# Kernel optimization log

Measured on AMD Instinct MI355X. Metric: run time of the kernel, lower is better.

Reference implementation:

```python
import jax, jax.numpy as jnp
import numpy as np
import math

L = 6      # num transformer layers
D = 128    # hidden_dim
H = 8      # heads
C = D // H # per-head dim (concat -> H*C == hidden_dim so residual add works)
F = 9      # node_features
OUT = 3    # output_dim
B, S, NN = 2, 128, 64
N = B * S * NN
E = 262144


def setup_inputs() -> dict:
    key = jax.random.key(0)
    ks = jax.random.split(key, 16)
    sc = 0.02
    g = lambda k, shp: jax.random.normal(k, shp, jnp.float32) * sc

    x = jax.random.normal(ks[0], (N, F), jnp.float32)
    edge_index = jax.random.randint(ks[1], (2, E), 0, N, dtype=jnp.int32)

    # sinusoidal positional encoding buffer [S, D]
    pos = np.arange(S, dtype=np.float32)[:, None]
    div = np.exp(np.arange(0, D, 2, dtype=np.float32) * (-math.log(10000.0) / D))
    pe = np.zeros((S, D), np.float32)
    pe[:, 0::2] = np.sin(pos * div)
    pe[:, 1::2] = np.cos(pos * div)

    return dict(
        x=x, edge_index=edge_index, pe=jnp.asarray(pe),
        Win=g(ks[2], (F, D)), bin_=jnp.zeros((D,), jnp.float32),
        Wq=g(ks[3], (L, D, D)), bq=jnp.zeros((L, D), jnp.float32),
        Wk=g(ks[4], (L, D, D)), bk=jnp.zeros((L, D), jnp.float32),
        Wv=g(ks[5], (L, D, D)), bv=jnp.zeros((L, D), jnp.float32),
        Ws=g(ks[6], (L, D, D)), bs=jnp.zeros((L, D), jnp.float32),
        Wb=g(ks[7], (L, 3 * D, 1)), bb=jnp.zeros((L, 1), jnp.float32),
        ln_g=jnp.ones((L, D), jnp.float32), ln_b=jnp.zeros((L, D), jnp.float32),
        Wo1=g(ks[8], (D, D // 2)), bo1=jnp.zeros((D // 2,), jnp.float32),
        Wo2=g(ks[9], (D // 2, OUT)), bo2=jnp.zeros((OUT,), jnp.float32),
        batch_size=B, seq_len=S, num_nodes=NN,
    )


def _layer_norm(x, g, b, eps=1e-5):
    mu = x.mean(-1, keepdims=True)
    var = ((x - mu) ** 2).mean(-1, keepdims=True)
    return (x - mu) / jnp.sqrt(var + eps) * g + b


def _transformer_conv(h, src, dst, Wq, bq, Wk, bk, Wv, bv, Ws, bs, Wb, bb):
    # PyG TransformerConv (beta=True, concat): edge gather -> per-head dot scores
    # -> scatter-softmax over incoming edges per dst node -> scatter-add aggregate.
    n = h.shape[0]
    q = (h @ Wq + bq).reshape(n, H, C)
    k = (h @ Wk + bk).reshape(n, H, C)
    v = (h @ Wv + bv).reshape(n, H, C)
    scores = jnp.einsum('ehc,ehc->eh', q[dst], k[src]) / math.sqrt(C)  # [E,H]
    m = jax.ops.segment_max(scores, dst, num_segments=n)               # [N,H]
    ex = jnp.exp(scores - jax.lax.stop_gradient(m)[dst])
    denom = jax.ops.segment_sum(ex, dst, num_segments=n)
    alpha = ex / (denom[dst] + 1e-16)                                  # [E,H]
    msg = (v[src] * alpha[:, :, None]).reshape(-1, H * C)              # [E,D]
    agg = jax.ops.segment_sum(msg, dst, num_segments=n)                # [N,D]
    xr = h @ Ws + bs                                                   # skip branch
    beta = jax.nn.sigmoid(jnp.concatenate([agg, xr, agg - xr], -1) @ Wb + bb)
    return beta * xr + (1.0 - beta) * agg


def reference(x, edge_index, pe, Win, bin_, Wq, bq, Wk, bk, Wv, bv, Ws, bs,
              Wb, bb, ln_g, ln_b, Wo1, bo1, Wo2, bo2,
              batch_size, seq_len, num_nodes):
    src, dst = edge_index[0], edge_index[1]
    d = Win.shape[1]
    h = x @ Win + bin_
    # add temporal positional encoding per timestep
    h = (h.reshape(batch_size, seq_len, num_nodes, d)
         + pe[:seq_len][None, :, None, :]).reshape(-1, d)
    for i in range(Wq.shape[0]):
        hn = _transformer_conv(h, src, dst, Wq[i], bq[i], Wk[i], bk[i],
                               Wv[i], bv[i], Ws[i], bs[i], Wb[i], bb[i])
        h = _layer_norm(h + hn, ln_g[i], ln_b[i])
    return jax.nn.relu(h @ Wo1 + bo1) @ Wo2 + bo2
```

## Files before the change

kernel.cpp:

```cpp
#include <hip/hip_runtime.h>

#define NNODES 16384
#define EDGES  262144
#define DH     128
#define NH     8
#define CH     16
#define NL     6
#define SEQ    128
#define NNPG   64

#define PBLK   768
#define PTHR   (PBLK * 256)
#define PWAV   (PBLK * 4)

typedef short bf16x8 __attribute__((ext_vector_type(8)));
typedef float f32x4 __attribute__((ext_vector_type(4)));
typedef float f32x2 __attribute__((ext_vector_type(2)));

static __device__ __forceinline__ unsigned short f2bf(float f) {
  unsigned u = __float_as_uint(f);
  u += 0x7FFFu + ((u >> 16) & 1u);
  return (unsigned short)(u >> 16);
}
static __device__ __forceinline__ float bfl(unsigned u) { return __uint_as_float(u << 16); }
static __device__ __forceinline__ float bfh(unsigned u) { return __uint_as_float(u & 0xffff0000u); }
static __device__ __forceinline__ f32x2 mk2(float x, float y) { f32x2 t; t[0] = x; t[1] = y; return t; }

__global__ __launch_bounds__(256) void k_pro(const int* __restrict__ ei,
    int* __restrict__ cnt, int* __restrict__ csr_pad,
    const float* __restrict__ Wq, const float* __restrict__ Wk,
    const float* __restrict__ Wv, const float* __restrict__ Ws,
    unsigned short* __restrict__ Wf,
    const float* __restrict__ x, const float* __restrict__ Win,
    const float* __restrict__ bin, const float* __restrict__ pe,
    float* __restrict__ h, unsigned short* __restrict__ hb) {
  const int tid = threadIdx.x;
  const int lane = tid & 63, wid = tid >> 6;
  const int gtid = blockIdx.x * 256 + tid;
  const int gw = blockIdx.x * 4 + wid;

  for (int e = gtid; e < EDGES; e += PTHR) {
    const int d = ei[EDGES + e];
    const int s = ei[e];
    const int slot = atomicAdd(&cnt[d], 1);
    if (slot < 64) csr_pad[d * 64 + (slot & 7) * 8 + (slot >> 3)] = s;
  }

  if (gw < NL * 128) {
    const int layer = gw >> 7, rem = gw & 127;
    const int mat = rem >> 5, tile = rem & 31;
    const int nt = tile >> 2, kt = tile & 3;
    const float* W = ((mat == 0) ? Wq : (mat == 1) ? Wk : (mat == 2) ? Wv : Ws)
                     + layer * DH * DH;
    const int nn = nt * 16 + (lane & 15);
    const int k0 = kt * 32 + (lane >> 4) * 8;
    unsigned pk[4];
#pragma unroll
    for (int jj = 0; jj < 4; ++jj) {
      const unsigned lo = f2bf(W[(k0 + 2 * jj) * DH + nn]);
      const unsigned hi = f2bf(W[(k0 + 2 * jj + 1) * DH + nn]);
      pk[jj] = lo | (hi << 16);
    }
    uint4 o = {pk[0], pk[1], pk[2], pk[3]};
    *(uint4*)&Wf[(((layer * 4 + mat) * 32 + tile) * 64 + lane) * 8] = o;
  }

  for (int n = gw; n < NNODES; n += PWAV) {
    const int d0 = lane * 2;
    float xs[9];
#pragma unroll
    for (int f = 0; f < 9; ++f) xs[f] = x[n * 9 + f];
    float a0 = bin[d0], a1 = bin[d0 + 1];
#pragma unroll
    for (int f = 0; f < 9; ++f) {
      const float2 w = *(const float2*)&Win[f * DH + d0];
      a0 = fmaf(xs[f], w.x, a0);
      a1 = fmaf(xs[f], w.y, a1);
    }
    const float2 pev = *(const float2*)&pe[((n / NNPG) % SEQ) * DH + d0];
    const float v0 = a0 + pev.x, v1 = a1 + pev.y;
    float2 hv = {v0, v1};
    *(float2*)&h[n * DH + d0] = hv;
    *(unsigned*)&hb[n * DH + d0] = (unsigned)f2bf(v0) | ((unsigned)f2bf(v1) << 16);
  }
}

__global__ __launch_bounds__(512, 2) void k_gemm(const unsigned short* __restrict__ hb,
    const unsigned short* __restrict__ Wf,
    const float* __restrict__ bq, const float* __restrict__ bk,
    const float* __restrict__ bv, const float* __restrict__ bs,
    unsigned short* __restrict__ qb, unsigned char* __restrict__ kv8,
    float* __restrict__ xr) {
  __shared__ uint4 As4[512];
  const int mt = blockIdx.x;
  const int wv = threadIdx.x >> 6, lane = threadIdx.x & 63;
  {
    const int t = threadIdx.x;
    const int row = t >> 4, cb = t & 15;
    As4[t] = *(const uint4*)&hb[(mt * 32 + row) * DH + ((cb ^ (row & 7)) * 8)];
  }
  __syncthreads();

  const int g = wv;
  const int mat = g >> 1, nbase = (g & 1) * 64;
  const unsigned short* Wm = Wf + mat * 16384;
  const float* bias = (mat == 0) ? bq : (mat == 1) ? bk : (mat == 2) ? bv : bs;
  const int m0 = lane & 15, quad = lane >> 4;
  const int nt0 = (g & 1) * 4;
  const char* Asb = (const char*)As4;

  const f32x4 z = {0.f, 0.f, 0.f, 0.f};
  f32x4 acc[2][4] = {{z, z, z, z}, {z, z, z, z}};
#pragma unroll
  for (int kt = 0; kt < 4; ++kt) {
    const int cbr = kt * 4 + quad;
    const bf16x8 a0 = *(const bf16x8*)(Asb + m0 * 256 + ((cbr ^ (m0 & 7)) * 16));
    const bf16x8 a1 = *(const bf16x8*)(Asb + (16 + m0) * 256 + ((cbr ^ (m0 & 7)) * 16));
#pragma unroll
    for (int j = 0; j < 4; ++j) {
      const bf16x8 b = *(const bf16x8*)&Wm[(((nt0 + j) * 4 + kt) * 64 + lane) * 8];
      acc[0][j] = __builtin_amdgcn_mfma_f32_16x16x32_bf16(a0, b, acc[0][j], 0, 0, 0);
      acc[1][j] = __builtin_amdgcn_mfma_f32_16x16x32_bf16(a1, b, acc[1][j], 0, 0, 0);
    }
  }
  const int kvoff = (mat == 1) ? 0 : 16;
#pragma unroll
  for (int half = 0; half < 2; ++half) {
#pragma unroll
    for (int j = 0; j < 4; ++j) {
      const int col = nbase + j * 16 + m0;
      const float bvv = bias[col];
#pragma unroll
      for (int r = 0; r < 4; ++r) {
        const float val = acc[half][j][r] + bvv;
        const int row = mt * 32 + half * 16 + quad * 4 + r;
        if (mat == 0) {
          qb[row * DH + col] = f2bf(val);
        } else if (mat == 3) {
          xr[row * DH + col] = val;
        } else {
          const float nbv = __shfl_xor(val, 1);
          if ((lane & 1) == 0) {
            const int pk = __builtin_amdgcn_cvt_pk_fp8_f32(val, nbv, 0, false);
            const int head = col >> 4, dim = col & 15;
            *(unsigned short*)&kv8[row * 256 + head * 32 + kvoff + dim] =
                (unsigned short)pk;
          }
        }
      }
    }
  }
}

__device__ __forceinline__ void load16bf2(const unsigned short* __restrict__ p, f32x2* r) {
  const uint4 a = *(const uint4*)p;
  const uint4 b = *(const uint4*)(p + 8);
  r[0] = mk2(bfl(a.x), bfh(a.x)); r[1] = mk2(bfl(a.y), bfh(a.y));
  r[2] = mk2(bfl(a.z), bfh(a.z)); r[3] = mk2(bfl(a.w), bfh(a.w));
  r[4] = mk2(bfl(b.x), bfh(b.x)); r[5] = mk2(bfl(b.y), bfh(b.y));
  r[6] = mk2(bfl(b.z), bfh(b.z)); r[7] = mk2(bfl(b.w), bfh(b.w));
}

__device__ __forceinline__ void decode8x2(const uint4 u, f32x2* r) {
  r[0] = __builtin_amdgcn_cvt_pk_f32_fp8(u.x, false);
  r[1] = __builtin_amdgcn_cvt_pk_f32_fp8(u.x, true);
  r[2] = __builtin_amdgcn_cvt_pk_f32_fp8(u.y, false);
  r[3] = __builtin_amdgcn_cvt_pk_f32_fp8(u.y, true);
  r[4] = __builtin_amdgcn_cvt_pk_f32_fp8(u.z, false);
  r[5] = __builtin_amdgcn_cvt_pk_f32_fp8(u.z, true);
  r[6] = __builtin_amdgcn_cvt_pk_f32_fp8(u.w, false);
  r[7] = __builtin_amdgcn_cvt_pk_f32_fp8(u.w, true);
}

__device__ __forceinline__ void edge_acc2(const uint4 ku, const uint4 vu, bool valid,
    const f32x2* __restrict__ q2, f32x2* __restrict__ a2, float& denom) {
  f32x2 kr[8];
  decode8x2(ku, kr);
  f32x2 d2 = mk2(0.f, 0.f);
#pragma unroll
  for (int c = 0; c < 8; ++c) d2 = d2 + q2[c] * kr[c];
  const float dot = d2[0] + d2[1];
  const float ex = valid ? __expf(dot * 0.25f) : 0.f;
  denom += ex;
  f32x2 vr[8];
  decode8x2(vu, vr);
  const f32x2 e2 = mk2(ex, ex);
#pragma unroll
  for (int c = 0; c < 8; ++c) a2[c] = a2[c] + e2 * vr[c];
}

__global__ __launch_bounds__(256, 4) void k_attn_epi(const unsigned short* __restrict__ qb,
    const unsigned char* __restrict__ kv8,
    const int* __restrict__ degv, const int* __restrict__ csr_pad,
    float* __restrict__ h, unsigned short* __restrict__ hb,
    const float* __restrict__ xr,
    const float* __restrict__ Wb, const float* __restrict__ bb,
    const float* __restrict__ ln_g, const float* __restrict__ ln_b) {
  const int wv = threadIdx.x >> 6, lane = threadIdx.x & 63;
  const int n = blockIdx.x * 4 + wv;
  const int es = lane >> 3, hd = lane & 7;
  const int4 iv = *(const int4*)&csr_pad[n * 64 + es * 8];
  const int deg = degv[n];
  const int ntb = min((deg + 7) >> 3, 8);
  const int idx[4] = {iv.x, iv.y, iv.z, iv.w};
  bool val[4];
#pragma unroll
  for (int t = 0; t < 4; ++t) val[t] = (es + 8 * t) < deg;
  f32x2 q2[8];
  load16bf2(&qb[n * DH + hd * CH], q2);
  const int d0 = hd * CH + es * 2;
  const float2 r = *(const float2*)&xr[n * DH + d0];
  const float2 hv = *(const float2*)&h[n * DH + d0];
  const float2 w0 = *(const float2*)&Wb[d0];
  const float2 w1 = *(const float2*)&Wb[DH + d0];
  const float2 w2 = *(const float2*)&Wb[2 * DH + d0];
  const float2 g = *(const float2*)&ln_g[d0];
  const float2 b = *(const float2*)&ln_b[d0];
  const float bbv = bb[0];
  uint4 kf[4], vf[4];
#pragma unroll
  for (int t = 0; t < 4; ++t) {
    if (t < ntb) {
      const int s = val[t] ? idx[t] : 0;
      const unsigned char* base = &kv8[s * 256 + hd * 32];
      kf[t] = *(const uint4*)base;
      vf[t] = *(const uint4*)(base + 16);
    }
  }
  f32x2 a2[8];
#pragma unroll
  for (int c = 0; c < 8; ++c) a2[c] = mk2(0.f, 0.f);
  float denom = 0.f;
#pragma unroll
  for (int t = 0; t < 4; ++t) {
    if (t < ntb) edge_acc2(kf[t], vf[t], val[t], q2, a2, denom);
  }
  for (int t = 4; t < ntb; ++t) {
    const bool v = (es + 8 * t) < deg;
    const int s = v ? csr_pad[n * 64 + es * 8 + t] : 0;
    const unsigned char* base = &kv8[s * 256 + hd * 32];
    const uint4 ku = *(const uint4*)base;
    const uint4 vu = *(const uint4*)(base + 16);
    edge_acc2(ku, vu, v, q2, a2, denom);
  }
#pragma unroll
  for (int off = 8; off <= 32; off <<= 1) denom += __shfl_xor(denom, off);
  const bool hi32 = (lane & 32) != 0;
  f32x2 r4[4];
#pragma unroll
  for (int c = 0; c < 4; ++c) {
    const f32x2 keep = hi32 ? a2[c + 4] : a2[c];
    const f32x2 send = hi32 ? a2[c] : a2[c + 4];
    const f32x2 rec = mk2(__shfl_xor(send[0], 32), __shfl_xor(send[1], 32));
    r4[c] = keep + rec;
  }
  const bool hi16 = (lane & 16) != 0;
  f32x2 r2[2];
#pragma unroll
  for (int c = 0; c < 2; ++c) {
    const f32x2 keep = hi16 ? r4[c + 2] : r4[c];
    const f32x2 send = hi16 ? r4[c] : r4[c + 2];
    const f32x2 rec = mk2(__shfl_xor(send[0], 16), __shfl_xor(send[1], 16));
    r2[c] = keep + rec;
  }
  const bool hi8 = (lane & 8) != 0;
  f32x2 rr;
  {
    const f32x2 keep = hi8 ? r2[1] : r2[0];
    const f32x2 send = hi8 ? r2[0] : r2[1];
    const f32x2 rec = mk2(__shfl_xor(send[0], 8), __shfl_xor(send[1], 8));
    rr = keep + rec;
  }
  const float inv = 1.f / (denom + 1e-16f);
  const float ax = rr[0] * inv, ay = rr[1] * inv;
  float p = ax * w0.x + ay * w0.y + r.x * w1.x + r.y * w1.y
          + (ax - r.x) * w2.x + (ay - r.y) * w2.y;
#pragma unroll
  for (int off = 1; off <= 32; off <<= 1) p += __shfl_xor(p, off);
  const float beta = 1.f / (1.f + __expf(-(p + bbv)));
  const float t0 = hv.x + beta * r.x + (1.f - beta) * ax;
  const float t1 = hv.y + beta * r.y + (1.f - beta) * ay;
  float sum = t0 + t1, sq = t0 * t0 + t1 * t1;
#pragma unroll
  for (int off = 1; off <= 32; off <<= 1) {
    sum += __shfl_xor(sum, off);
    sq  += __shfl_xor(sq, off);
  }
  const float mu = sum * (1.f / DH);
  const float rinv = rsqrtf(sq * (1.f / DH) - mu * mu + 1e-5f);
  float2 o = {(t0 - mu) * rinv * g.x + b.x, (t1 - mu) * rinv * g.y + b.y};
  *(float2*)&h[n * DH + d0] = o;
  *(unsigned*)&hb[n * DH + d0] = (unsigned)f2bf(o.x) | ((unsigned)f2bf(o.y) << 16);
}

__global__ __launch_bounds__(256) void k_final(const float* __restrict__ h,
    const float* __restrict__ Wo1, const float* __restrict__ bo1,
    const float* __restrict__ Wo2, const float* __restrict__ bo2,
    float* __restrict__ out) {
  __shared__ float hs[4][DH];
  const int lane = threadIdx.x & 63, wid = threadIdx.x >> 6;
  const int n = blockIdx.x * 4 + wid;
  const float2 hv = *(const float2*)&h[n * DH + lane * 2];
  hs[wid][lane * 2] = hv.x;
  hs[wid][lane * 2 + 1] = hv.y;
  float m = bo1[lane];
#pragma unroll 16
  for (int d = 0; d < DH; ++d) m = fmaf(hs[wid][d], Wo1[d * 64 + lane], m);
  m = fmaxf(m, 0.f);
  float o0 = m * Wo2[lane * 3 + 0];
  float o1 = m * Wo2[lane * 3 + 1];
  float o2 = m * Wo2[lane * 3 + 2];
#pragma unroll
  for (int off = 32; off; off >>= 1) {
    o0 += __shfl_xor(o0, off);
    o1 += __shfl_xor(o1, off);
    o2 += __shfl_xor(o2, off);
  }
  if (lane == 0) {
    out[n * 3 + 0] = o0 + bo2[0];
    out[n * 3 + 1] = o1 + bo2[1];
    out[n * 3 + 2] = o2 + bo2[2];
  }
}

extern "C" void kernel_launch(void* const* d_in, const int* in_sizes, int n_in,
                              void* d_out, int out_size, void* d_ws, size_t ws_size,
                              hipStream_t stream) {
  const float* x   = (const float*)d_in[0];
  const int*   ei  = (const int*)d_in[1];
  const float* pe  = (const float*)d_in[2];
  const float* Win = (const float*)d_in[3];
  const float* bin = (const float*)d_in[4];
  const float* Wq  = (const float*)d_in[5];
  const float* bq  = (const float*)d_in[6];
  const float* Wk  = (const float*)d_in[7];
  const float* bk  = (const float*)d_in[8];
  const float* Wv  = (const float*)d_in[9];
  const float* bv  = (const float*)d_in[10];
  const float* Wsk = (const float*)d_in[11];
  const float* bs  = (const float*)d_in[12];
  const float* Wb  = (const float*)d_in[13];
  const float* bb  = (const float*)d_in[14];
  const float* lng = (const float*)d_in[15];
  const float* lnb = (const float*)d_in[16];
  const float* Wo1 = (const float*)d_in[17];
  const float* bo1 = (const float*)d_in[18];
  const float* Wo2 = (const float*)d_in[19];
  const float* bo2 = (const float*)d_in[20];

  const size_t NU = (size_t)NNODES * DH;
  char* base = (char*)d_ws;
  float* h   = (float*)base;                  base += NU * 4;
  float* xr  = (float*)base;                  base += NU * 4;
  unsigned short* hb = (unsigned short*)base; base += NU * 2;
  unsigned short* qb = (unsigned short*)base; base += NU * 2;
  unsigned char* kv8 = (unsigned char*)base;  base += NU * 2;
  unsigned short* Wf = (unsigned short*)base; base += (size_t)NL * 4 * 16384 * 2;
  int* cnt       = (int*)base;                base += NNODES * 4;
  int* csr_pad   = (int*)base;                base += (size_t)NNODES * 64 * 4;

  (void)hipMemsetAsync(cnt, 0, NNODES * sizeof(int), stream);
  k_pro<<<PBLK, 256, 0, stream>>>(ei, cnt, csr_pad, Wq, Wk, Wv, Wsk, Wf,
                                  x, Win, bin, pe, h, hb);
  for (int l = 0; l < NL; ++l) {
    k_gemm<<<NNODES / 32, 512, 0, stream>>>(
        hb, Wf + (size_t)l * 4 * 16384,
        bq + l * DH, bk + l * DH, bv + l * DH, bs + l * DH, qb, kv8, xr);
    k_attn_epi<<<NNODES / 4, 256, 0, stream>>>(qb, kv8, cnt, csr_pad,
                                               h, hb, xr, Wb + l * 3 * DH, bb + l,
                                               lng + l * DH, lnb + l * DH);
  }
  k_final<<<NNODES / 4, 256, 0, stream>>>(h, Wo1, bo1, Wo2, bo2, (float*)d_out);
}
```

Measured before the change: 332.3 us.

## Fuse attention epilogue with next layer's QKVS GEMM via ping-pong buffers

Merges each layer's attention/LayerNorm epilogue with the following layer's projection GEMM in one kernel. The normalized rows go straight into swizzled shared memory as bf16 and feed the MFMA GEMM, so the hb round trip and a kernel launch per layer disappear. q/kv/xr are double-buffered so the next layer's outputs don't overwrite inputs other blocks are still gathering. The last layer also fuses the output MLP. The cost is fewer, larger blocks (512 threads handling 32 nodes serially, 4 per wave), which may reduce latency hiding for the irregular edge gathers.

```diff
diff --git a/kernel.cpp b/kernel.cpp
--- a/kernel.cpp
+++ b/kernel.cpp
@@ -101,12 +101,12 @@
   }
   __syncthreads();
 
-  const int g = wv;
-  const int mat = g >> 1, nbase = (g & 1) * 64;
+  const int cg = wv;
+  const int mat = cg >> 1, nbase = (cg & 1) * 64;
   const unsigned short* Wm = Wf + mat * 16384;
   const float* bias = (mat == 0) ? bq : (mat == 1) ? bk : (mat == 2) ? bv : bs;
   const int m0 = lane & 15, quad = lane >> 4;
-  const int nt0 = (g & 1) * 4;
+  const int nt0 = (cg & 1) * 4;
   const char* Asb = (const char*)As4;
 
   const f32x4 z = {0.f, 0.f, 0.f, 0.f};
@@ -189,137 +189,204 @@
   for (int c = 0; c < 8; ++c) a2[c] = a2[c] + e2 * vr[c];
 }
 
-__global__ __launch_bounds__(256, 4) void k_attn_epi(const unsigned short* __restrict__ qb,
-    const unsigned char* __restrict__ kv8,
+template <bool LAST>
+__global__ __launch_bounds__(512, 2) void k_layer(
+    const unsigned short* __restrict__ qb_i, const unsigned char* __restrict__ kv8_i,
     const int* __restrict__ degv, const int* __restrict__ csr_pad,
-    float* __restrict__ h, unsigned short* __restrict__ hb,
-    const float* __restrict__ xr,
+    float* __restrict__ h, const float* __restrict__ xr_i,
     const float* __restrict__ Wb, const float* __restrict__ bb,
-    const float* __restrict__ ln_g, const float* __restrict__ ln_b) {
-  const int wv = threadIdx.x >> 6, lane = threadIdx.x & 63;
-  const int n = blockIdx.x * 4 + wv;
-  const int es = lane >> 3, hd = lane & 7;
-  const int4 iv = *(const int4*)&csr_pad[n * 64 + es * 8];
-  const int deg = degv[n];
-  const int ntb = min((deg + 7) >> 3, 8);
-  const int idx[4] = {iv.x, iv.y, iv.z, iv.w};
-  bool val[4];
-#pragma unroll
-  for (int t = 0; t < 4; ++t) val[t] = (es + 8 * t) < deg;
-  f32x2 q2[8];
-  load16bf2(&qb[n * DH + hd * CH], q2);
-  const int d0 = hd * CH + es * 2;
-  const float2 r = *(const float2*)&xr[n * DH + d0];
-  const float2 hv = *(const float2*)&h[n * DH + d0];
-  const float2 w0 = *(const float2*)&Wb[d0];
-  const float2 w1 = *(const float2*)&Wb[DH + d0];
-  const float2 w2 = *(const float2*)&Wb[2 * DH + d0];
-  const float2 g = *(const float2*)&ln_g[d0];
-  const float2 b = *(const float2*)&ln_b[d0];
-  const float bbv = bb[0];
-  uint4 kf[4], vf[4];
-#pragma unroll
-  for (int t = 0; t < 4; ++t) {
-    if (t < ntb) {
-      const int s = val[t] ? idx[t] : 0;
-      const unsigned char* base = &kv8[s * 256 + hd * 32];
-      kf[t] = *(const uint4*)base;
-      vf[t] = *(const uint4*)(base + 16);
-    }
-  }
-  f32x2 a2[8];
-#pragma unroll
-  for (int c = 0; c < 8; ++c) a2[c] = mk2(0.f, 0.f);
-  float denom = 0.f;
-#pragma unroll
-  for (int t = 0; t < 4; ++t) {
-    if (t < ntb) edge_acc2(kf[t], vf[t], val[t], q2, a2, denom);
-  }
-  for (int t = 4; t < ntb; ++t) {
-    const bool v = (es + 8 * t) < deg;
-    const int s = v ? csr_pad[n * 64 + es * 8 + t] : 0;
-    const unsigned char* base = &kv8[s * 256 + hd * 32];
-    const uint4 ku = *(const uint4*)base;
-    const uint4 vu = *(const uint4*)(base + 16);
-    edge_acc2(ku, vu, v, q2, a2, denom);
-  }
-#pragma unroll
-  for (int off = 8; off <= 32; off <<= 1) denom += __shfl_xor(denom, off);
-  const bool hi32 = (lane & 32) != 0;
-  f32x2 r4[4];
-#pragma unroll
-  for (int c = 0; c < 4; ++c) {
-    const f32x2 keep = hi32 ? a2[c + 4] : a2[c];
-    const f32x2 send = hi32 ? a2[c] : a2[c + 4];
-    const f32x2 rec = mk2(__shfl_xor(send[0], 32), __shfl_xor(send[1], 32));
-    r4[c] = keep + rec;
-  }
-  const bool hi16 = (lane & 16) != 0;
-  f32x2 r2[2];
-#pragma unroll
-  for (int c = 0; c < 2; ++c) {
-    const f32x2 keep = hi16 ? r4[c + 2] : r4[c];
-    const f32x2 send = hi16 ? r4[c] : r4[c + 2];
-    const f32x2 rec = mk2(__shfl_xor(send[0], 16), __shfl_xor(send[1], 16));
-    r2[c] = keep + rec;
-  }
-  const bool hi8 = (lane & 8) != 0;
-  f32x2 rr;
-  {
-    const f32x2 keep = hi8 ? r2[1] : r2[0];
-    const f32x2 send = hi8 ? r2[0] : r2[1];
-    const f32x2 rec = mk2(__shfl_xor(send[0], 8), __shfl_xor(send[1], 8));
-    rr = keep + rec;
-  }
-  const float inv = 1.f / (denom + 1e-16f);
-  const float ax = rr[0] * inv, ay = rr[1] * inv;
-  float p = ax * w0.x + ay * w0.y + r.x * w1.x + r.y * w1.y
-          + (ax - r.x) * w2.x + (ay - r.y) * w2.y;
-#pragma unroll
-  for (int off = 1; off <= 32; off <<= 1) p += __shfl_xor(p, off);
-  const float beta = 1.f / (1.f + __expf(-(p + bbv)));
-  const float t0 = hv.x + beta * r.x + (1.f - beta) * ax;
-  const float t1 = hv.y + beta * r.y + (1.f - beta) * ay;
-  float sum = t0 + t1, sq = t0 * t0 + t1 * t1;
-#pragma unroll
-  for (int off = 1; off <= 32; off <<= 1) {
-    sum += __shfl_xor(sum, off);
-    sq  += __shfl_xor(sq, off);
-  }
-  const float mu = sum * (1.f / DH);
-  const float rinv = rsqrtf(sq * (1.f / DH) - mu * mu + 1e-5f);
-  float2 o = {(t0 - mu) * rinv * g.x + b.x, (t1 - mu) * rinv * g.y + b.y};
-  *(float2*)&h[n * DH + d0] = o;
-  *(unsigned*)&hb[n * DH + d0] = (unsigned)f2bf(o.x) | ((unsigned)f2bf(o.y) << 16);
-}
-
-__global__ __launch_bounds__(256) void k_final(const float* __restrict__ h,
+    const float* __restrict__ ln_g, const float* __restrict__ ln_b,
+    const unsigned short* __restrict__ Wfn, const float* __restrict__ bqn,
+    const float* __restrict__ bkn, const float* __restrict__ bvn,
+    const float* __restrict__ bsn,
+    unsigned short* __restrict__ qb_o, unsigned char* __restrict__ kv8_o,
+    float* __restrict__ xr_o,
     const float* __restrict__ Wo1, const float* __restrict__ bo1,
     const float* __restrict__ Wo2, const float* __restrict__ bo2,
     float* __restrict__ out) {
-  __shared__ float hs[4][DH];
-  const int lane = threadIdx.x & 63, wid = threadIdx.x >> 6;
-  const int n = blockIdx.x * 4 + wid;
-  const float2 hv = *(const float2*)&h[n * DH + lane * 2];
-  hs[wid][lane * 2] = hv.x;
-  hs[wid][lane * 2 + 1] = hv.y;
-  float m = bo1[lane];
+  __shared__ float hsf[32][DH];
+  const int wv = threadIdx.x >> 6, lane = threadIdx.x & 63;
+  const int nb = blockIdx.x * 32;
+  const int es = lane >> 3, hd = lane & 7;
+  const int d0 = hd * CH + es * 2;
+  const float2 lw0 = *(const float2*)&Wb[d0];
+  const float2 lw1 = *(const float2*)&Wb[DH + d0];
+  const float2 lw2 = *(const float2*)&Wb[2 * DH + d0];
+  const float2 lg = *(const float2*)&ln_g[d0];
+  const float2 lb = *(const float2*)&ln_b[d0];
+  const float bbv = bb[0];
+
+  for (int t4 = 0; t4 < 4; ++t4) {
+    const int row = wv * 4 + t4;
+    const int n = nb + row;
+    const int4 iv = *(const int4*)&csr_pad[n * 64 + es * 8];
+    const int deg = degv[n];
+    int ntb = (deg + 7) >> 3;
+    if (ntb > 8) ntb = 8;
+    const int idx[4] = {iv.x, iv.y, iv.z, iv.w};
+    bool valv[4];
+#pragma unroll
+    for (int t = 0; t < 4; ++t) valv[t] = (es + 8 * t) < deg;
+    f32x2 q2[8];
+    load16bf2(&qb_i[n * DH + hd * CH], q2);
+    const float2 xrv = *(const float2*)&xr_i[n * DH + d0];
+    const float2 hv = *(const float2*)&h[n * DH + d0];
+    uint4 kf[4], vf[4];
+#pragma unroll
+    for (int t = 0; t < 4; ++t) {
+      if (t < ntb) {
+        const int s = valv[t] ? idx[t] : 0;
+        const unsigned char* base = &kv8_i[s * 256 + hd * 32];
+        kf[t] = *(const uint4*)base;
+        vf[t] = *(const uint4*)(base + 16);
+      }
+    }
+    f32x2 a2[8];
+#pragma unroll
+    for (int c = 0; c < 8; ++c) a2[c] = mk2(0.f, 0.f);
+    float denom = 0.f;
+#pragma unroll
+    for (int t = 0; t < 4; ++t) {
+      if (t < ntb) edge_acc2(kf[t], vf[t], valv[t], q2, a2, denom);
+    }
+    for (int t = 4; t < ntb; ++t) {
+      const bool v = (es + 8 * t) < deg;
+      const int s = v ? csr_pad[n * 64 + es * 8 + t] : 0;
+      const unsigned char* base = &kv8_i[s * 256 + hd * 32];
+      const uint4 ku = *(const uint4*)base;
+      const uint4 vu = *(const uint4*)(base + 16);
+      edge_acc2(ku, vu, v, q2, a2, denom);
+    }
+#pragma unroll
+    for (int off = 8; off <= 32; off <<= 1) denom += __shfl_xor(denom, off);
+    const bool hi32 = (lane & 32) != 0;
+    f32x2 r4[4];
+#pragma unroll
+    for (int c = 0; c < 4; ++c) {
+      const f32x2 keep = hi32 ? a2[c + 4] : a2[c];
+      const f32x2 send = hi32 ? a2[c] : a2[c + 4];
+      const f32x2 rec = mk2(__shfl_xor(send[0], 32), __shfl_xor(send[1], 32));
+      r4[c] = keep + rec;
+    }
+    const bool hi16 = (lane & 16) != 0;
+    f32x2 r2[2];
+#pragma unroll
+    for (int c = 0; c < 2; ++c) {
+      const f32x2 keep = hi16 ? r4[c + 2] : r4[c];
+      const f32x2 send = hi16 ? r4[c] : r4[c + 2];
+      const f32x2 rec = mk2(__shfl_xor(send[0], 16), __shfl_xor(send[1], 16));
+      r2[c] = keep + rec;
+    }
+    const bool hi8 = (lane & 8) != 0;
+    f32x2 rr;
+    {
+      const f32x2 keep = hi8 ? r2[1] : r2[0];
+      const f32x2 send = hi8 ? r2[0] : r2[1];
+      const f32x2 rec = mk2(__shfl_xor(send[0], 8), __shfl_xor(send[1], 8));
+      rr = keep + rec;
+    }
+    const float inv = 1.f / (denom + 1e-16f);
+    const float ax = rr[0] * inv, ay = rr[1] * inv;
+    float p = ax * lw0.x + ay * lw0.y + xrv.x * lw1.x + xrv.y * lw1.y
+            + (ax - xrv.x) * lw2.x + (ay - xrv.y) * lw2.y;
+#pragma unroll
+    for (int off = 1; off <= 32; off <<= 1) p += __shfl_xor(p, off);
+    const float beta = 1.f / (1.f + __expf(-(p + bbv)));
+    const float t0 = hv.x + beta * xrv.x + (1.f - beta) * ax;
+    const float t1 = hv.y + beta * xrv.y + (1.f - beta) * ay;
+    float sum = t0 + t1, sq = t0 * t0 + t1 * t1;
+#pragma unroll
+    for (int off = 1; off <= 32; off <<= 1) {
+      sum += __shfl_xor(sum, off);
+      sq  += __shfl_xor(sq, off);
+    }
+    const float mu = sum * (1.f / DH);
+    const float rinv = rsqrtf(sq * (1.f / DH) - mu * mu + 1e-5f);
+    const float2 o = {(t0 - mu) * rinv * lg.x + lb.x, (t1 - mu) * rinv * lg.y + lb.y};
+    if constexpr (!LAST) {
+      *(float2*)&h[n * DH + d0] = o;
+      const int cb = 2 * hd + (es >> 2);
+      *(unsigned*)((char*)hsf + row * 256 + ((cb ^ (row & 7)) * 16) + (es & 3) * 4) =
+          (unsigned)f2bf(o.x) | ((unsigned)f2bf(o.y) << 16);
+    } else {
+      hsf[row][d0] = o.x;
+      hsf[row][d0 + 1] = o.y;
+    }
+  }
+  __syncthreads();
+
+  if constexpr (!LAST) {
+    const int cg = wv;
+    const int mat = cg >> 1, nbase = (cg & 1) * 64;
+    const unsigned short* Wm = Wfn + mat * 16384;
+    const float* bias = (mat == 0) ? bqn : (mat == 1) ? bkn : (mat == 2) ? bvn : bsn;
+    const int m0 = lane & 15, quad = lane >> 4;
+    const int nt0 = (cg & 1) * 4;
+    const char* Asb = (const char*)hsf;
+    const f32x4 z = {0.f, 0.f, 0.f, 0.f};
+    f32x4 acc[2][4] = {{z, z, z, z}, {z, z, z, z}};
+#pragma unroll
+    for (int kt = 0; kt < 4; ++kt) {
+      const int cbr = kt * 4 + quad;
+      const bf16x8 a0 = *(const bf16x8*)(Asb + m0 * 256 + ((cbr ^ (m0 & 7)) * 16));
+      const bf16x8 a1 = *(const bf16x8*)(Asb + (16 + m0) * 256 + ((cbr ^ (m0 & 7)) * 16));
+#pragma unroll
+      for (int j = 0; j < 4; ++j) {
+        const bf16x8 b = *(const bf16x8*)&Wm[(((nt0 + j) * 4 + kt) * 64 + lane) * 8];
+        acc[0][j] = __builtin_amdgcn_mfma_f32_16x16x32_bf16(a0, b, acc[0][j], 0, 0, 0);
+        acc[1][j] = __builtin_amdgcn_mfma_f32_16x16x32_bf16(a1, b, acc[1][j], 0, 0, 0);
+      }
+    }
+    const int kvoff = (mat == 1) ? 0 : 16;
+#pragma unroll
+    for (int half = 0; half < 2; ++half) {
+#pragma unroll
+      for (int j = 0; j < 4; ++j) {
+        const int col = nbase + j * 16 + m0;
+        const float bvv = bias[col];
+#pragma unroll
+        for (int r = 0; r < 4; ++r) {
+          const float val = acc[half][j][r] + bvv;
+          const int row = nb + half * 16 + quad * 4 + r;
+          if (mat == 0) {
+            qb_o[row * DH + col] = f2bf(val);
+          } else if (mat == 3) {
+            xr_o[row * DH + col] = val;
+          } else {
+            const float nbv = __shfl_xor(val, 1);
+            if ((lane & 1) == 0) {
+              const int pk = __builtin_amdgcn_cvt_pk_fp8_f32(val, nbv, 0, false);
+              const int head = col >> 4, dim = col & 15;
+              *(unsigned short*)&kv8_o[row * 256 + head * 32 + kvoff + dim] =
+                  (unsigned short)pk;
+            }
+          }
+        }
+      }
+    }
+  } else {
+    for (int t4 = 0; t4 < 4; ++t4) {
+      const int row = wv * 4 + t4;
+      const int n = nb + row;
+      float m = bo1[lane];
 #pragma unroll 16
-  for (int d = 0; d < DH; ++d) m = fmaf(hs[wid][d], Wo1[d * 64 + lane], m);
-  m = fmaxf(m, 0.f);
-  float o0 = m * Wo2[lane * 3 + 0];
-  float o1 = m * Wo2[lane * 3 + 1];
-  float o2 = m * Wo2[lane * 3 + 2];
-#pragma unroll
-  for (int off = 32; off; off >>= 1) {
-    o0 += __shfl_xor(o0, off);
-    o1 += __shfl_xor(o1, off);
-    o2 += __shfl_xor(o2, off);
-  }
-  if (lane == 0) {
-    out[n * 3 + 0] = o0 + bo2[0];
-    out[n * 3 + 1] = o1 + bo2[1];
-    out[n * 3 + 2] = o2 + bo2[2];
+      for (int d = 0; d < DH; ++d) m = fmaf(hsf[row][d], Wo1[d * 64 + lane], m);
+      m = fmaxf(m, 0.f);
+      float o0 = m * Wo2[lane * 3 + 0];
+      float o1 = m * Wo2[lane * 3 + 1];
+      float o2 = m * Wo2[lane * 3 + 2];
+#pragma unroll
+      for (int off = 32; off; off >>= 1) {
+        o0 += __shfl_xor(o0, off);
+        o1 += __shfl_xor(o1, off);
+        o2 += __shfl_xor(o2, off);
+      }
+      if (lane == 0) {
+        out[n * 3 + 0] = o0 + bo2[0];
+        out[n * 3 + 1] = o1 + bo2[1];
+        out[n * 3 + 2] = o2 + bo2[2];
+      }
+    }
   }
 }
 
@@ -351,24 +418,34 @@
   const size_t NU = (size_t)NNODES * DH;
   char* base = (char*)d_ws;
   float* h   = (float*)base;                  base += NU * 4;
-  float* xr  = (float*)base;                  base += NU * 4;
   unsigned short* hb = (unsigned short*)base; base += NU * 2;
-  unsigned short* qb = (unsigned short*)base; base += NU * 2;
-  unsigned char* kv8 = (unsigned char*)base;  base += NU * 2;
   unsigned short* Wf = (unsigned short*)base; base += (size_t)NL * 4 * 16384 * 2;
-  int* cnt       = (int*)base;                base += NNODES * 4;
-  int* csr_pad   = (int*)base;                base += (size_t)NNODES * 64 * 4;
+  int* cnt     = (int*)base;                  base += NNODES * 4;
+  int* csr_pad = (int*)base;                  base += (size_t)NNODES * 64 * 4;
+  float* xrA = (float*)base;                  base += NU * 4;
+  float* xrB = (float*)base;                  base += NU * 4;
+  unsigned short* qbA = (unsigned short*)base; base += NU * 2;
+  unsigned short* qbB = (unsigned short*)base; base += NU * 2;
+  unsigned char* kvA = (unsigned char*)base;  base += NU * 2;
+  unsigned char* kvB = (unsigned char*)base;  base += NU * 2;
 
   (void)hipMemsetAsync(cnt, 0, NNODES * sizeof(int), stream);
   k_pro<<<PBLK, 256, 0, stream>>>(ei, cnt, csr_pad, Wq, Wk, Wv, Wsk, Wf,
                                   x, Win, bin, pe, h, hb);
-  for (int l = 0; l < NL; ++l) {
-    k_gemm<<<NNODES / 32, 512, 0, stream>>>(
-        hb, Wf + (size_t)l * 4 * 16384,
-        bq + l * DH, bk + l * DH, bv + l * DH, bs + l * DH, qb, kv8, xr);
-    k_attn_epi<<<NNODES / 4, 256, 0, stream>>>(qb, kv8, cnt, csr_pad,
-                                               h, hb, xr, Wb + l * 3 * DH, bb + l,
-                                               lng + l * DH, lnb + l * DH);
-  }
-  k_final<<<NNODES / 4, 256, 0, stream>>>(h, Wo1, bo1, Wo2, bo2, (float*)d_out);
-}
+  k_gemm<<<NNODES / 32, 512, 0, stream>>>(hb, Wf, bq, bk, bv, bs, qbA, kvA, xrA);
+  for (int l = 0; l < NL - 1; ++l) {
+    const bool even = (l & 1) == 0;
+    k_layer<false><<<NNODES / 32, 512, 0, stream>>>(
+        even ? qbA : qbB, even ? kvA : kvB, cnt, csr_pad, h, even ? xrA : xrB,
+        Wb + l * 3 * DH, bb + l, lng + l * DH, lnb + l * DH,
+        Wf + (size_t)(l + 1) * 4 * 16384,
+        bq + (l + 1) * DH, bk + (l + 1) * DH, bv + (l + 1) * DH, bs + (l + 1) * DH,
+        even ? qbB : qbA, even ? kvB : kvA, even ? xrB : xrA,
+        Wo1, bo1, Wo2, bo2, (float*)d_out);
+  }
+  k_layer<true><<<NNODES / 32, 512, 0, stream>>>(
+      qbB, kvB, cnt, csr_pad, h, xrB,
+      Wb + 5 * 3 * DH, bb + 5, lng + 5 * DH, lnb + 5 * DH,
+      Wf, bq, bk, bv, bs, qbA, kvA, xrA,
+      Wo1, bo1, Wo2, bo2, (float*)d_out);
+}
```

After: 331.2 us. About the same (-0.3%).
